# Performance work log

Hardware: AMD Instinct MI355X
Metric: run time of the kernel (lower is better)

The kernel has to match this reference:

```python
import jax, jax.numpy as jnp
import numpy as np
from jax import lax


def _binarize(t):
    # sign binarization to +1/-1 (zero maps to -1, matching torch.where(t > 0, 1, -1))
    return jnp.where(t > 0, 1.0, -1.0).astype(t.dtype)


def _bconv(x, w, b):
    # binary conv: binarize input and weights, then standard 3x3 'same' conv
    y = lax.conv_general_dilated(
        _binarize(x), _binarize(w),
        window_strides=(1, 1), padding=((1, 1), (1, 1)),
        dimension_numbers=('NCHW', 'OIHW', 'NCHW'))
    return y + b[None, :, None, None]


def _maxpool2(x):
    return lax.reduce_window(x, -jnp.inf, lax.max, (1, 1, 2, 2), (1, 1, 2, 2), 'VALID')


def setup_inputs() -> dict:
    key = jax.random.key(0)
    ks = jax.random.split(key, 13)
    s = 0.1
    return {
        'x': jax.random.normal(ks[0], (4096, 1, 28, 28), jnp.float32),
        'w1': jax.random.normal(ks[1], (32, 1, 3, 3), jnp.float32) * s,
        'b1': jax.random.normal(ks[2], (32,), jnp.float32) * s,
        'w2': jax.random.normal(ks[3], (64, 32, 3, 3), jnp.float32) * s,
        'b2': jax.random.normal(ks[4], (64,), jnp.float32) * s,
        'w3': jax.random.normal(ks[5], (16, 64, 3, 3), jnp.float32) * s,
        'b3': jax.random.normal(ks[6], (16,), jnp.float32) * s,
        'fc1_w': jax.random.normal(ks[7], (256, 16 * 7 * 7), jnp.float32) * s,
        'fc1_b': jax.random.normal(ks[8], (256,), jnp.float32) * s,
        'fc2_w': jax.random.normal(ks[9], (128, 256), jnp.float32) * s,
        'fc2_b': jax.random.normal(ks[10], (128,), jnp.float32) * s,
        'fc3_w': jax.random.normal(ks[11], (10, 128), jnp.float32) * s,
        'fc3_b': jax.random.normal(ks[12], (10,), jnp.float32) * s,
    }


def reference(x, w1, b1, w2, b2, w3, b3, fc1_w, fc1_b, fc2_w, fc2_b, fc3_w, fc3_b):
    h = jax.nn.relu(_maxpool2(_bconv(x, w1, b1)))      # [B,32,14,14]
    h = jax.nn.relu(_maxpool2(_bconv(h, w2, b2)))      # [B,64,7,7]
    h = jax.nn.relu(_bconv(h, w3, b3))                 # [B,16,7,7]
    h = h.reshape(-1, 16 * 7 * 7)
    h = jax.nn.relu(h @ fc1_w.T + fc1_b)
    h = jax.nn.relu(h @ fc2_w.T + fc2_b)
    return h @ fc3_w.T + fc3_b                          # [B,10]
```

## Files before the change

### kernel.cpp

```cpp
#include <hip/hip_runtime.h>
#include <cstdint>

#define OFF_PW    0
#define OFF_W1T   4096
#define OFF_W2T   823296
#define OFF_H3T   954368
#define OFF_H1T   14061568
#define OFF_H2T   18255872

__global__ __launch_bounds__(256) void prep(
    const float* __restrict__ w1, const float* __restrict__ w2,
    const float* __restrict__ w3,
    const float* __restrict__ fc1_w, const float* __restrict__ fc2_w,
    uint32_t* __restrict__ pw, float* __restrict__ w1T,
    float* __restrict__ w2T, float* __restrict__ h3T) {
    int idx = blockIdx.x * 256 + threadIdx.x;
    if (idx < 204800) {
        int k = idx >> 8, n = idx & 255;
        w1T[idx] = (k < 784) ? fc1_w[n * 784 + k] : 0.f;
        return;
    }
    idx -= 204800;
    if (idx < 32768) {
        int k = idx >> 7, n = idx & 127;
        w2T[idx] = fc2_w[n * 256 + k];
        return;
    }
    idx -= 32768;
    if (idx < 65536) {
        h3T[784 * 4096 + idx] = 0.f;
        return;
    }
    idx -= 65536;
    if (idx >= 896) return;
    if (idx < 32) {
        uint32_t b = 0;
#pragma unroll
        for (int k = 0; k < 9; ++k) b |= (w1[idx * 9 + k] > 0.f ? 1u : 0u) << k;
        pw[idx] = b;
    } else if (idx < 608) {
        int e = idx - 32;
        int oc = e / 9, tap = e - oc * 9;
        uint32_t b = 0;
#pragma unroll
        for (int ic = 0; ic < 32; ++ic)
            b |= (w2[(oc * 32 + ic) * 9 + tap] > 0.f ? 1u : 0u) << ic;
        pw[idx] = b;
    } else {
        int e = idx - 608;
        int oc = e / 18, r = e - oc * 18;
        int tap = r >> 1, half = r & 1;
        uint32_t b = 0;
#pragma unroll
        for (int ic = 0; ic < 32; ++ic)
            b |= (w3[(oc * 64 + half * 32 + ic) * 9 + tap] > 0.f ? 1u : 0u) << ic;
        pw[idx] = b;
    }
}

__device__ __forceinline__ uint32_t bfe3(uint32_t r, int j) { return (r >> j) & 7u; }

__global__ __launch_bounds__(256, 2) void conv_stack(
    const float* __restrict__ x, const float* __restrict__ b1,
    const float* __restrict__ b2, const float* __restrict__ b3,
    const uint32_t* __restrict__ pw, float* __restrict__ h3T) {
    __shared__ uint32_t s_xr[8 * 36];
    __shared__ uint32_t s_H1[8 * 260];
    __shared__ uint32_t s_H2[8 * 164];
    __shared__ uint32_t s_w1[32];
    __shared__ int s_sth1[32], s_ic1[32], s_ic2[64];
    __shared__ uint32_t s_W2t[576];
    __shared__ uint32_t s_W3t[288];
    __shared__ float s_b3[16];

    const int t = threadIdx.x;
    const int lane = t & 63;
    const int wid = t >> 6;
    const int img0 = blockIdx.x * 8;

    for (int i = t; i < 8 * 260; i += 256) s_H1[i] = 0;
    for (int i = t; i < 8 * 164; i += 256) s_H2[i] = 0;
    if (t < 224) {
        int im = t / 28, row = t - im * 28;
        const float4* xr = (const float4*)(x + (img0 + im) * 784 + row * 28);
        uint32_t b = 0;
#pragma unroll
        for (int q = 0; q < 7; ++q) {
            float4 v = xr[q];
            b |= (v.x > 0.f ? 1u : 0u) << (q * 4 + 0);
            b |= (v.y > 0.f ? 1u : 0u) << (q * 4 + 1);
            b |= (v.z > 0.f ? 1u : 0u) << (q * 4 + 2);
            b |= (v.w > 0.f ? 1u : 0u) << (q * 4 + 3);
        }
        s_xr[im * 36 + row] = b << 1;
    }
    if (t < 32) {
        s_w1[t] = pw[t];
        int ic = (int)floorf(-b1[t]) + 1;
        s_ic1[t] = ic;
        s_sth1[t] = (9 - ic) >> 1;
    } else if (t >= 32 && t < 96) {
        s_ic2[t - 32] = (int)floorf(-b2[t - 32]) + 1;
    } else if (t >= 96 && t < 112) {
        s_b3[t - 96] = b3[t - 96];
    }
    for (int i = t; i < 576; i += 256)
        s_W2t[i] = pw[32 + (i & 63) * 9 + (i >> 6)];
    for (int i = t; i < 288; i += 256)
        s_W3t[i] = pw[608 + (i & 15) * 18 + (i >> 4)];
    __syncthreads();

    for (int task = t; task < 1568; task += 256) {
        int pid = task >> 3, im = task & 7;
        int pi, pj;
        if (pid < 144) { pi = 1 + pid / 12; pj = 1 + pid - (pid / 12) * 12; }
        else {
            int b = pid - 144;
            if (b < 14)      { pi = 0;  pj = b; }
            else if (b < 28) { pi = 13; pj = b - 14; }
            else if (b < 40) { pi = 1 + (b - 28); pj = 0; }
            else             { pi = 1 + (b - 40); pj = 13; }
        }
        const uint32_t* xr = &s_xr[im * 36];
        int y0 = 2 * pi - 1;
        uint32_t r0 = (pi > 0)  ? xr[y0]     : 0u;
        uint32_t r1 = xr[y0 + 1];
        uint32_t r2 = xr[y0 + 2];
        uint32_t r3 = (pi < 13) ? xr[y0 + 3] : 0u;
        int j0 = 2 * pj, j1 = 2 * pj + 1;
        uint32_t s00 = bfe3(r0, j0) | (bfe3(r1, j0) << 3) | (bfe3(r2, j0) << 6);
        uint32_t s01 = bfe3(r0, j1) | (bfe3(r1, j1) << 3) | (bfe3(r2, j1) << 6);
        uint32_t s10 = bfe3(r1, j0) | (bfe3(r2, j0) << 3) | (bfe3(r3, j0) << 6);
        uint32_t s11 = bfe3(r1, j1) | (bfe3(r2, j1) << 3) | (bfe3(r3, j1) << 6);
        uint32_t word = 0;
        if (pid < 144) {
#pragma unroll
            for (int c = 0; c < 32; ++c) {
                uint32_t w = s_w1[c];
                int S = min(min(__popc(s00 ^ w), __popc(s01 ^ w)),
                            min(__popc(s10 ^ w), __popc(s11 ^ w)));
                word |= (uint32_t)(S <= s_sth1[c]) << c;
            }
        } else {
            uint32_t iT = (pi == 0)  ? 0x7u   : 0u;
            uint32_t iB = (pi == 13) ? 0x1C0u : 0u;
            uint32_t iL = (pj == 0)  ? 0x49u  : 0u;
            uint32_t iR = (pj == 13) ? 0x124u : 0u;
            uint32_t i00 = iT | iL, i01 = iT | iR, i10 = iB | iL, i11 = iB | iR;
            int n00 = 9 - __popc(i00), n01 = 9 - __popc(i01);
            int n10 = 9 - __popc(i10), n11 = 9 - __popc(i11);
#pragma unroll
            for (int c = 0; c < 32; ++c) {
                uint32_t w = s_w1[c];
                int v0 = n00 - 2 * (__popc(s00 ^ w) - __popc(w & i00));
                int v1 = n01 - 2 * (__popc(s01 ^ w) - __popc(w & i01));
                int v2 = n10 - 2 * (__popc(s10 ^ w) - __popc(w & i10));
                int v3 = n11 - 2 * (__popc(s11 ^ w) - __popc(w & i11));
                int vm = max(max(v0, v1), max(v2, v3));
                word |= (uint32_t)(vm >= s_ic1[c]) << c;
            }
        }
        s_H1[im * 260 + (pi + 1) * 16 + (pj + 1)] = word;
    }
    __syncthreads();

    {
        uint32_t w0 = s_W2t[0 * 64 + lane], w1r = s_W2t[1 * 64 + lane],
                 w2r = s_W2t[2 * 64 + lane], w3r = s_W2t[3 * 64 + lane],
                 w4 = s_W2t[4 * 64 + lane], w5 = s_W2t[5 * 64 + lane],
                 w6 = s_W2t[6 * 64 + lane], w7 = s_W2t[7 * 64 + lane],
                 w8 = s_W2t[8 * 64 + lane];
        int ic2 = s_ic2[lane];
        int sth2 = (288 - ic2) >> 1;
        int pc0 = __popc(w0), pc1 = __popc(w1r), pc2 = __popc(w2r);
        int pc3 = __popc(w3r), pc5 = __popc(w5), pc6 = __popc(w6);
        int pc7 = __popc(w7), pc8 = __popc(w8);
        int topc = pc0 + pc1 + pc2, botc = pc6 + pc7 + pc8;
        int lefc = pc0 + pc3 + pc6, rigc = pc2 + pc5 + pc8;

        for (int wt = wid; wt < 392; wt += 4) {
            int im = wt & 7, pos = wt >> 3;
            int pi, pj;
            if (pos < 25) { pi = 1 + pos / 5; pj = 1 + pos - (pos / 5) * 5; }
            else {
                int b = pos - 25;
                if (b < 7)       { pi = 0; pj = b; }
                else if (b < 14) { pi = 6; pj = b - 7; }
                else if (b < 19) { pi = b - 13; pj = 0; }
                else             { pi = b - 18; pj = 6; }
            }
            int base = im * 260 + 2 * pi * 16 + 2 * pj;
            uint2 ra0 = *(const uint2*)&s_H1[base],      ra1 = *(const uint2*)&s_H1[base + 2];
            uint2 rb0 = *(const uint2*)&s_H1[base + 16], rb1 = *(const uint2*)&s_H1[base + 18];
            uint2 rc0 = *(const uint2*)&s_H1[base + 32], rc1 = *(const uint2*)&s_H1[base + 34];
            uint2 rd0 = *(const uint2*)&s_H1[base + 48], rd1 = *(const uint2*)&s_H1[base + 50];
            uint32_t c00 = ra0.x, c01 = ra0.y, c02 = ra1.x, c03 = ra1.y;
            uint32_t c10 = rb0.x, c11 = rb0.y, c12 = rb1.x, c13 = rb1.y;
            uint32_t c20 = rc0.x, c21 = rc0.y, c22 = rc1.x, c23 = rc1.y;
            uint32_t c30 = rd0.x, c31 = rd0.y, c32 = rd1.x, c33 = rd1.y;
            int S00 = __popc(c00 ^ w0) + __popc(c01 ^ w1r) + __popc(c02 ^ w2r)
                    + __popc(c10 ^ w3r) + __popc(c11 ^ w4) + __popc(c12 ^ w5)
                    + __popc(c20 ^ w6) + __popc(c21 ^ w7) + __popc(c22 ^ w8);
            int S01 = __popc(c01 ^ w0) + __popc(c02 ^ w1r) + __popc(c03 ^ w2r)
                    + __popc(c11 ^ w3r) + __popc(c12 ^ w4) + __popc(c13 ^ w5)
                    + __popc(c21 ^ w6) + __popc(c22 ^ w7) + __popc(c23 ^ w8);
            int S10 = __popc(c10 ^ w0) + __popc(c11 ^ w1r) + __popc(c12 ^ w2r)
                    + __popc(c20 ^ w3r) + __popc(c21 ^ w4) + __popc(c22 ^ w5)
                    + __popc(c30 ^ w6) + __popc(c31 ^ w7) + __popc(c32 ^ w8);
            int S11 = __popc(c11 ^ w0) + __popc(c12 ^ w1r) + __popc(c13 ^ w2r)
                    + __popc(c21 ^ w3r) + __popc(c22 ^ w4) + __popc(c23 ^ w5)
                    + __popc(c31 ^ w6) + __popc(c32 ^ w7) + __popc(c33 ^ w8);
            int pred;
            if (pos < 25) {
                int Sm = min(min(S00, S01), min(S10, S11));
                pred = (Sm <= sth2);
            } else {
                int vmax;
                {
                    int rI = (pi == 0), cI = (pj == 0);
                    int corr = (rI ? topc : 0) + (cI ? lefc : 0) - ((rI & cI) ? pc0 : 0);
                    int nv = 32 * (9 - 3 * rI - 3 * cI + (rI & cI));
                    vmax = nv - 2 * (S00 - corr);
                }
                {
                    int rI = (pi == 0), cI = (pj == 6);
                    int corr = (rI ? topc : 0) + (cI ? rigc : 0) - ((rI & cI) ? pc2 : 0);
                    int nv = 32 * (9 - 3 * rI - 3 * cI + (rI & cI));
                    vmax = max(vmax, nv - 2 * (S01 - corr));
                }
                {
                    int rI = (pi == 6), cI = (pj == 0);
                    int corr = (rI ? botc : 0) + (cI ? lefc : 0) - ((rI & cI) ? pc6 : 0);
                    int nv = 32 * (9 - 3 * rI - 3 * cI + (rI & cI));
                    vmax = max(vmax, nv - 2 * (S10 - corr));
                }
                {
                    int rI = (pi == 6), cI = (pj == 6);
                    int corr = (rI ? botc : 0) + (cI ? rigc : 0) - ((rI & cI) ? pc8 : 0);
                    int nv = 32 * (9 - 3 * rI - 3 * cI + (rI & cI));
                    vmax = max(vmax, nv - 2 * (S11 - corr));
                }
                pred = (vmax >= ic2);
            }
            unsigned long long m = __ballot(pred);
            if (lane == 0) {
                *(uint2*)&s_H2[im * 164 + ((pi + 1) * 9 + (pj + 1)) * 2] =
                    make_uint2((uint32_t)m, (uint32_t)(m >> 32));
            }
        }
    }
    __syncthreads();

    {
        int oc = lane & 15, iq = lane >> 4;
        uint32_t w[18];
#pragma unroll
        for (int k = 0; k < 18; ++k) w[k] = s_W3t[k * 16 + oc];
        float bias3 = s_b3[oc];
        int pc[9];
#pragma unroll
        for (int k = 0; k < 9; ++k) pc[k] = __popc(w[2 * k]) + __popc(w[2 * k + 1]);
        int topc = pc[0] + pc[1] + pc[2], botc = pc[6] + pc[7] + pc[8];
        int lefc = pc[0] + pc[3] + pc[6], rigc = pc[2] + pc[5] + pc[8];

        for (int wt = wid; wt < 98; wt += 4) {
            int iq2 = wt & 1, pos = wt >> 1;
            int im = iq2 * 4 + iq;
            int pi, pj;
            if (pos < 25) { pi = 1 + pos / 5; pj = 1 + pos - (pos / 5) * 5; }
            else {
                int b = pos - 25;
                if (b < 7)       { pi = 0; pj = b; }
                else if (b < 14) { pi = 6; pj = b - 7; }
                else if (b < 19) { pi = b - 13; pj = 0; }
                else             { pi = b - 18; pj = 6; }
            }
            const uint32_t* hp = &s_H2[im * 164];
            int S = 0;
#pragma unroll
            for (int kh = 0; kh < 3; ++kh)
#pragma unroll
                for (int kw = 0; kw < 3; ++kw) {
                    uint2 cc = *(const uint2*)&hp[((pi + kh) * 9 + (pj + kw)) * 2];
                    int k = kh * 3 + kw;
                    S += __popc(cc.x ^ w[2 * k]) + __popc(cc.y ^ w[2 * k + 1]);
                }
            int v;
            if (pos < 25) {
                v = 576 - 2 * S;
            } else {
                int rT = (pi == 0), rB = (pi == 6), cL = (pj == 0), cR = (pj == 6);
                int rA = rT | rB, cA = cL | cR;
                int corr = (rT ? topc : 0) + (rB ? botc : 0) +
                           (cL ? lefc : 0) + (cR ? rigc : 0);
                if (rT & cL) corr -= pc[0];
                if (rT & cR) corr -= pc[2];
                if (rB & cL) corr -= pc[6];
                if (rB & cR) corr -= pc[8];
                int nInv = 3 * rA + 3 * cA - (rA & cA);
                v = 64 * (9 - nInv) - 2 * (S - corr);
            }
            float h = fmaxf((float)v + bias3, 0.f);
            h3T[(oc * 49 + pi * 7 + pj) * 4096 + img0 + im] = h;
        }
    }
}

__global__ __launch_bounds__(256, 2) void fc1_gemm(
    const float* __restrict__ aT, const float* __restrict__ bT,
    const float* __restrict__ bias, float* __restrict__ oT) {
    const int LDA = 68, LDB = 36;
    __shared__ float As[160 * LDA];
    __shared__ float Bs[160 * LDB];
    const int t = threadIdx.x;
    const int tx = t & 15, ty = t >> 4;
    const int img0 = blockIdx.x * 64;
    const int n0 = blockIdx.y * 32;
    float acc[4][2] = {{0.f}};

    for (int kc = 0; kc < 800; kc += 160) {
#pragma unroll
        for (int s = 0; s < 10; ++s) {
            int v = t + s * 256;
            int kk = v >> 4, q = (v & 15) * 4;
            *(float4*)&As[kk * LDA + q] =
                *(const float4*)&aT[(kc + kk) * 4096 + img0 + q];
        }
#pragma unroll
        for (int s = 0; s < 5; ++s) {
            int v = t + s * 256;
            int kk = v >> 3, q = (v & 7) * 4;
            *(float4*)&Bs[kk * LDB + q] =
                *(const float4*)&bT[(kc + kk) * 256 + n0 + q];
        }
        __syncthreads();
#pragma unroll 8
        for (int kk = 0; kk < 160; ++kk) {
            float4 a = *(const float4*)&As[kk * LDA + ty * 4];
            float2 b = *(const float2*)&Bs[kk * LDB + tx * 2];
            acc[0][0] += a.x * b.x; acc[0][1] += a.x * b.y;
            acc[1][0] += a.y * b.x; acc[1][1] += a.y * b.y;
            acc[2][0] += a.z * b.x; acc[2][1] += a.z * b.y;
            acc[3][0] += a.w * b.x; acc[3][1] += a.w * b.y;
        }
        __syncthreads();
    }
#pragma unroll
    for (int j = 0; j < 2; ++j) {
        int n = n0 + tx * 2 + j;
        float bj = bias[n];
        float4 ov;
        ov.x = fmaxf(acc[0][j] + bj, 0.f);
        ov.y = fmaxf(acc[1][j] + bj, 0.f);
        ov.z = fmaxf(acc[2][j] + bj, 0.f);
        ov.w = fmaxf(acc[3][j] + bj, 0.f);
        *(float4*)&oT[n * 4096 + img0 + ty * 4] = ov;
    }
}

__global__ __launch_bounds__(256, 2) void fc2_gemm(
    const float* __restrict__ aT, const float* __restrict__ bT,
    const float* __restrict__ bias, float* __restrict__ oT) {
    const int LD = 36;
    __shared__ float As[256 * LD];
    __shared__ float Bs[256 * LD];
    const int t = threadIdx.x;
    const int tx = t & 15, ty = t >> 4;
    const int img0 = blockIdx.x * 32;
    const int n0 = blockIdx.y * 32;
    float acc[2][2] = {{0.f}};

#pragma unroll
    for (int s = 0; s < 8; ++s) {
        int v = t + s * 256;
        int kk = v >> 3, q = (v & 7) * 4;
        *(float4*)&As[kk * LD + q] = *(const float4*)&aT[kk * 4096 + img0 + q];
        *(float4*)&Bs[kk * LD + q] = *(const float4*)&bT[kk * 128 + n0 + q];
    }
    __syncthreads();
#pragma unroll 8
    for (int kk = 0; kk < 256; ++kk) {
        float2 a = *(const float2*)&As[kk * LD + ty * 2];
        float2 b = *(const float2*)&Bs[kk * LD + tx * 2];
        acc[0][0] += a.x * b.x; acc[0][1] += a.x * b.y;
        acc[1][0] += a.y * b.x; acc[1][1] += a.y * b.y;
    }
#pragma unroll
    for (int j = 0; j < 2; ++j) {
        int n = n0 + tx * 2 + j;
        float bj = bias[n];
        float2 ov;
        ov.x = fmaxf(acc[0][j] + bj, 0.f);
        ov.y = fmaxf(acc[1][j] + bj, 0.f);
        *(float2*)&oT[n * 4096 + img0 + ty * 2] = ov;
    }
}

__global__ __launch_bounds__(256) void fc3_gemm(
    const float* __restrict__ aT, const float* __restrict__ w,
    const float* __restrict__ bias, float* __restrict__ out) {
    int id = blockIdx.x * 256 + threadIdx.x;
    int n = id >> 12, img = id & 4095;
    const float* wr = w + n * 128;
    float a0 = 0.f, a1 = 0.f, a2 = 0.f, a3 = 0.f;
#pragma unroll 8
    for (int k = 0; k < 128; k += 4) {
        a0 += aT[(k + 0) * 4096 + img] * wr[k + 0];
        a1 += aT[(k + 1) * 4096 + img] * wr[k + 1];
        a2 += aT[(k + 2) * 4096 + img] * wr[k + 2];
        a3 += aT[(k + 3) * 4096 + img] * wr[k + 3];
    }
    out[img * 10 + n] = (a0 + a1) + (a2 + a3) + bias[n];
}

extern "C" void kernel_launch(void* const* d_in, const int* in_sizes, int n_in,
                              void* d_out, int out_size, void* d_ws, size_t ws_size,
                              hipStream_t stream) {
    const float* x     = (const float*)d_in[0];
    const float* w1    = (const float*)d_in[1];
    const float* b1    = (const float*)d_in[2];
    const float* w2    = (const float*)d_in[3];
    const float* b2    = (const float*)d_in[4];
    const float* w3    = (const float*)d_in[5];
    const float* b3    = (const float*)d_in[6];
    const float* fc1_w = (const float*)d_in[7];
    const float* fc1_b = (const float*)d_in[8];
    const float* fc2_w = (const float*)d_in[9];
    const float* fc2_b = (const float*)d_in[10];
    const float* fc3_w = (const float*)d_in[11];
    const float* fc3_b = (const float*)d_in[12];
    float* out = (float*)d_out;

    const int B = in_sizes[0] / 784;
    char* ws = (char*)d_ws;
    uint32_t* pw = (uint32_t*)(ws + OFF_PW);
    float* w1T = (float*)(ws + OFF_W1T);
    float* w2T = (float*)(ws + OFF_W2T);
    float* h3T = (float*)(ws + OFF_H3T);
    float* h1T = (float*)(ws + OFF_H1T);
    float* h2T = (float*)(ws + OFF_H2T);

    hipLaunchKernelGGL(prep, dim3(1188), dim3(256), 0, stream,
                       w1, w2, w3, fc1_w, fc2_w, pw, w1T, w2T, h3T);
    hipLaunchKernelGGL(conv_stack, dim3(B / 8), dim3(256), 0, stream,
                       x, b1, b2, b3, pw, h3T);
    hipLaunchKernelGGL(fc1_gemm, dim3(B / 64, 8), dim3(256), 0, stream,
                       h3T, w1T, fc1_b, h1T);
    hipLaunchKernelGGL(fc2_gemm, dim3(B / 32, 4), dim3(256), 0, stream,
                       h1T, w2T, fc2_b, h2T);
    hipLaunchKernelGGL(fc3_gemm, dim3(B * 10 / 256), dim3(256), 0, stream,
                       h2T, fc3_w, fc3_b, out);
}
```

Baseline: 224.9 us.

## Restructure conv stack per-image and split-K FC GEMMs with fused bias/ReLU epilogues

The conv stack now handles 4 images per block with one wavefront per image in layer 2. That wave loads whole H1 rows into registers and sweeps all 7 columns, replacing the per-position gather, and occupancy is raised to 4 blocks per CU. fc1 and fc2 become larger-register-tile split-K GEMMs that write partial sums into extra workspace buffers, or use atomics when the workspace is too small. The partial reduction, bias and ReLU are folded into the next layer's load. This aims to raise parallelism and data reuse in the GEMMs, but it adds partial-buffer traffic and a workspace-size-dependent code path.

After: 224.4 us. No clear change (-0.2%).

```diff
diff --git a/kernel.cpp b/kernel.cpp
--- a/kernel.cpp
+++ b/kernel.cpp
@@ -7,6 +7,9 @@
 #define OFF_H3T   954368
 #define OFF_H1T   14061568
 #define OFF_H2T   18255872
+#define OFF_H1EXT 20353024ull
+#define OFF_H2EXT 32935936ull
+#define WS_NEED_EXT 35033088ull
 
 __global__ __launch_bounds__(256) void prep(
     const float* __restrict__ w1, const float* __restrict__ w2,
@@ -60,28 +63,42 @@
 
 __device__ __forceinline__ uint32_t bfe3(uint32_t r, int j) { return (r >> j) & 7u; }
 
-__global__ __launch_bounds__(256, 2) void conv_stack(
+__global__ __launch_bounds__(256, 4) void conv_stack(
     const float* __restrict__ x, const float* __restrict__ b1,
     const float* __restrict__ b2, const float* __restrict__ b3,
     const uint32_t* __restrict__ pw, float* __restrict__ h3T) {
-    __shared__ uint32_t s_xr[8 * 36];
-    __shared__ uint32_t s_H1[8 * 260];
-    __shared__ uint32_t s_H2[8 * 164];
+    __shared__ __align__(16) uint32_t s_H1[4][16][16];
+    __shared__ __align__(16) uint32_t s_H2[4][9][9][2];
+    __shared__ uint32_t s_xr[4][32];
     __shared__ uint32_t s_w1[32];
     __shared__ int s_sth1[32], s_ic1[32], s_ic2[64];
-    __shared__ uint32_t s_W2t[576];
-    __shared__ uint32_t s_W3t[288];
+    __shared__ uint32_t s_W2t[9][64];
+    __shared__ uint32_t s_W3t[18][16];
     __shared__ float s_b3[16];
 
     const int t = threadIdx.x;
     const int lane = t & 63;
     const int wid = t >> 6;
-    const int img0 = blockIdx.x * 8;
-
-    for (int i = t; i < 8 * 260; i += 256) s_H1[i] = 0;
-    for (int i = t; i < 8 * 164; i += 256) s_H2[i] = 0;
-    if (t < 224) {
-        int im = t / 28, row = t - im * 28;
+    const int img0 = blockIdx.x * 4;
+
+    {
+        uint32_t* h1f = &s_H1[0][0][0];
+        for (int i = t; i < 1024; i += 256) h1f[i] = 0;
+        uint32_t* h2f = &s_H2[0][0][0][0];
+        for (int i = t; i < 648; i += 256) h2f[i] = 0;
+    }
+    if (t < 32) {
+        s_w1[t] = pw[t];
+        int ic = (int)floorf(-b1[t]) + 1;
+        s_ic1[t] = ic;
+        s_sth1[t] = (9 - ic) >> 1;
+    } else if (t < 96) {
+        s_ic2[t - 32] = (int)floorf(-b2[t - 32]) + 1;
+    } else if (t < 112) {
+        s_b3[t - 96] = b3[t - 96];
+    } else if (t >= 128 && t < 240) {
+        int r = t - 128;
+        int im = r / 28, row = r - im * 28;
         const float4* xr = (const float4*)(x + (img0 + im) * 784 + row * 28);
         uint32_t b = 0;
 #pragma unroll
@@ -92,26 +109,16 @@
             b |= (v.z > 0.f ? 1u : 0u) << (q * 4 + 2);
             b |= (v.w > 0.f ? 1u : 0u) << (q * 4 + 3);
         }
-        s_xr[im * 36 + row] = b << 1;
-    }
-    if (t < 32) {
-        s_w1[t] = pw[t];
-        int ic = (int)floorf(-b1[t]) + 1;
-        s_ic1[t] = ic;
-        s_sth1[t] = (9 - ic) >> 1;
-    } else if (t >= 32 && t < 96) {
-        s_ic2[t - 32] = (int)floorf(-b2[t - 32]) + 1;
-    } else if (t >= 96 && t < 112) {
-        s_b3[t - 96] = b3[t - 96];
+        s_xr[im][row] = b << 1;
     }
     for (int i = t; i < 576; i += 256)
-        s_W2t[i] = pw[32 + (i & 63) * 9 + (i >> 6)];
+        s_W2t[i >> 6][i & 63] = pw[32 + (i & 63) * 9 + (i >> 6)];
     for (int i = t; i < 288; i += 256)
-        s_W3t[i] = pw[608 + (i & 15) * 18 + (i >> 4)];
+        s_W3t[i >> 4][i & 15] = pw[608 + (i & 15) * 18 + (i >> 4)];
     __syncthreads();
 
-    for (int task = t; task < 1568; task += 256) {
-        int pid = task >> 3, im = task & 7;
+    for (int task = t; task < 784; task += 256) {
+        int im = task & 3, pid = task >> 2;
         int pi, pj;
         if (pid < 144) { pi = 1 + pid / 12; pj = 1 + pid - (pid / 12) * 12; }
         else {
@@ -121,7 +128,7 @@
             else if (b < 40) { pi = 1 + (b - 28); pj = 0; }
             else             { pi = 1 + (b - 40); pj = 13; }
         }
-        const uint32_t* xr = &s_xr[im * 36];
+        const uint32_t* xr = &s_xr[im][0];
         int y0 = 2 * pi - 1;
         uint32_t r0 = (pi > 0)  ? xr[y0]     : 0u;
         uint32_t r1 = xr[y0 + 1];
@@ -134,7 +141,7 @@
         uint32_t s11 = bfe3(r1, j1) | (bfe3(r2, j1) << 3) | (bfe3(r3, j1) << 6);
         uint32_t word = 0;
         if (pid < 144) {
-#pragma unroll
+#pragma unroll 4
             for (int c = 0; c < 32; ++c) {
                 uint32_t w = s_w1[c];
                 int S = min(min(__popc(s00 ^ w), __popc(s01 ^ w)),
@@ -149,7 +156,7 @@
             uint32_t i00 = iT | iL, i01 = iT | iR, i10 = iB | iL, i11 = iB | iR;
             int n00 = 9 - __popc(i00), n01 = 9 - __popc(i01);
             int n10 = 9 - __popc(i10), n11 = 9 - __popc(i11);
-#pragma unroll
+#pragma unroll 4
             for (int c = 0; c < 32; ++c) {
                 uint32_t w = s_w1[c];
                 int v0 = n00 - 2 * (__popc(s00 ^ w) - __popc(w & i00));
@@ -160,102 +167,102 @@
                 word |= (uint32_t)(vm >= s_ic1[c]) << c;
             }
         }
-        s_H1[im * 260 + (pi + 1) * 16 + (pj + 1)] = word;
+        s_H1[im][pi + 1][pj + 1] = word;
     }
     __syncthreads();
 
     {
-        uint32_t w0 = s_W2t[0 * 64 + lane], w1r = s_W2t[1 * 64 + lane],
-                 w2r = s_W2t[2 * 64 + lane], w3r = s_W2t[3 * 64 + lane],
-                 w4 = s_W2t[4 * 64 + lane], w5 = s_W2t[5 * 64 + lane],
-                 w6 = s_W2t[6 * 64 + lane], w7 = s_W2t[7 * 64 + lane],
-                 w8 = s_W2t[8 * 64 + lane];
+        const int im = wid;
+        uint32_t wv[9];
+#pragma unroll
+        for (int k = 0; k < 9; ++k) wv[k] = s_W2t[k][lane];
         int ic2 = s_ic2[lane];
         int sth2 = (288 - ic2) >> 1;
-        int pc0 = __popc(w0), pc1 = __popc(w1r), pc2 = __popc(w2r);
-        int pc3 = __popc(w3r), pc5 = __popc(w5), pc6 = __popc(w6);
-        int pc7 = __popc(w7), pc8 = __popc(w8);
-        int topc = pc0 + pc1 + pc2, botc = pc6 + pc7 + pc8;
-        int lefc = pc0 + pc3 + pc6, rigc = pc2 + pc5 + pc8;
-
-        for (int wt = wid; wt < 392; wt += 4) {
-            int im = wt & 7, pos = wt >> 3;
-            int pi, pj;
-            if (pos < 25) { pi = 1 + pos / 5; pj = 1 + pos - (pos / 5) * 5; }
-            else {
-                int b = pos - 25;
-                if (b < 7)       { pi = 0; pj = b; }
-                else if (b < 14) { pi = 6; pj = b - 7; }
-                else if (b < 19) { pi = b - 13; pj = 0; }
-                else             { pi = b - 18; pj = 6; }
+        int pc0 = __popc(wv[0]), pc2 = __popc(wv[2]);
+        int pc6 = __popc(wv[6]), pc8 = __popc(wv[8]);
+        int topc = pc0 + __popc(wv[1]) + pc2;
+        int botc = pc6 + __popc(wv[7]) + pc8;
+        int lefc = pc0 + __popc(wv[3]) + pc6;
+        int rigc = pc2 + __popc(wv[5]) + pc8;
+        const uint32_t* plane = &s_H1[im][0][0];
+
+        for (int pi = 0; pi < 7; ++pi) {
+            uint32_t C[4][16];
+#pragma unroll
+            for (int r = 0; r < 4; ++r) {
+                const uint32_t* rp = &plane[(2 * pi + r) * 16];
+                *(uint4*)&C[r][0]  = *(const uint4*)&rp[0];
+                *(uint4*)&C[r][4]  = *(const uint4*)&rp[4];
+                *(uint4*)&C[r][8]  = *(const uint4*)&rp[8];
+                *(uint4*)&C[r][12] = *(const uint4*)&rp[12];
             }
-            int base = im * 260 + 2 * pi * 16 + 2 * pj;
-            uint2 ra0 = *(const uint2*)&s_H1[base],      ra1 = *(const uint2*)&s_H1[base + 2];
-            uint2 rb0 = *(const uint2*)&s_H1[base + 16], rb1 = *(const uint2*)&s_H1[base + 18];
-            uint2 rc0 = *(const uint2*)&s_H1[base + 32], rc1 = *(const uint2*)&s_H1[base + 34];
-            uint2 rd0 = *(const uint2*)&s_H1[base + 48], rd1 = *(const uint2*)&s_H1[base + 50];
-            uint32_t c00 = ra0.x, c01 = ra0.y, c02 = ra1.x, c03 = ra1.y;
-            uint32_t c10 = rb0.x, c11 = rb0.y, c12 = rb1.x, c13 = rb1.y;
-            uint32_t c20 = rc0.x, c21 = rc0.y, c22 = rc1.x, c23 = rc1.y;
-            uint32_t c30 = rd0.x, c31 = rd0.y, c32 = rd1.x, c33 = rd1.y;
-            int S00 = __popc(c00 ^ w0) + __popc(c01 ^ w1r) + __popc(c02 ^ w2r)
-                    + __popc(c10 ^ w3r) + __popc(c11 ^ w4) + __popc(c12 ^ w5)
-                    + __popc(c20 ^ w6) + __popc(c21 ^ w7) + __popc(c22 ^ w8);
-            int S01 = __popc(c01 ^ w0) + __popc(c02 ^ w1r) + __popc(c03 ^ w2r)
-                    + __popc(c11 ^ w3r) + __popc(c12 ^ w4) + __popc(c13 ^ w5)
-                    + __popc(c21 ^ w6) + __popc(c22 ^ w7) + __popc(c23 ^ w8);
-            int S10 = __popc(c10 ^ w0) + __popc(c11 ^ w1r) + __popc(c12 ^ w2r)
-                    + __popc(c20 ^ w3r) + __popc(c21 ^ w4) + __popc(c22 ^ w5)
-                    + __popc(c30 ^ w6) + __popc(c31 ^ w7) + __popc(c32 ^ w8);
-            int S11 = __popc(c11 ^ w0) + __popc(c12 ^ w1r) + __popc(c13 ^ w2r)
-                    + __popc(c21 ^ w3r) + __popc(c22 ^ w4) + __popc(c23 ^ w5)
-                    + __popc(c31 ^ w6) + __popc(c32 ^ w7) + __popc(c33 ^ w8);
-            int pred;
-            if (pos < 25) {
-                int Sm = min(min(S00, S01), min(S10, S11));
-                pred = (Sm <= sth2);
-            } else {
-                int vmax;
-                {
-                    int rI = (pi == 0), cI = (pj == 0);
-                    int corr = (rI ? topc : 0) + (cI ? lefc : 0) - ((rI & cI) ? pc0 : 0);
-                    int nv = 32 * (9 - 3 * rI - 3 * cI + (rI & cI));
-                    vmax = nv - 2 * (S00 - corr);
+            const int rT = (pi == 0), rB = (pi == 6);
+#pragma unroll
+            for (int pj = 0; pj < 7; ++pj) {
+                int S00 = 0, S01 = 0, S10 = 0, S11 = 0;
+#pragma unroll
+                for (int kh = 0; kh < 3; ++kh)
+#pragma unroll
+                    for (int kw = 0; kw < 3; ++kw) {
+                        uint32_t ww = wv[kh * 3 + kw];
+                        S00 += __popc(C[kh][2 * pj + kw] ^ ww);
+                        S01 += __popc(C[kh][2 * pj + 1 + kw] ^ ww);
+                        S10 += __popc(C[kh + 1][2 * pj + kw] ^ ww);
+                        S11 += __popc(C[kh + 1][2 * pj + 1 + kw] ^ ww);
+                    }
+                int pred;
+                if (pj >= 1 && pj <= 5) {
+                    if (!rT && !rB) {
+                        int Sm = min(min(S00, S01), min(S10, S11));
+                        pred = (Sm <= sth2);
+                    } else if (rT) {
+                        int v0 = 192 - 2 * (S00 - topc);
+                        int v1 = 192 - 2 * (S01 - topc);
+                        int v2 = 288 - 2 * S10;
+                        int v3 = 288 - 2 * S11;
+                        pred = (max(max(v0, v1), max(v2, v3)) >= ic2);
+                    } else {
+                        int v0 = 288 - 2 * S00;
+                        int v1 = 288 - 2 * S01;
+                        int v2 = 192 - 2 * (S10 - botc);
+                        int v3 = 192 - 2 * (S11 - botc);
+                        pred = (max(max(v0, v1), max(v2, v3)) >= ic2);
+                    }
+                } else {
+                    const int cL = (pj == 0), cR = (pj == 6);
+                    int v0, v1, v2, v3;
+                    { int rI = rT, cI = cL;
+                      int corr = (rI ? topc : 0) + (cI ? lefc : 0) - ((rI & cI) ? pc0 : 0);
+                      int nv = 32 * (9 - 3 * rI - 3 * cI + (rI & cI));
+                      v0 = nv - 2 * (S00 - corr); }
+                    { int rI = rT, cI = cR;
+                      int corr = (rI ? topc : 0) + (cI ? rigc : 0) - ((rI & cI) ? pc2 : 0);
+                      int nv = 32 * (9 - 3 * rI - 3 * cI + (rI & cI));
+                      v1 = nv - 2 * (S01 - corr); }
+                    { int rI = rB, cI = cL;
+                      int corr = (rI ? botc : 0) + (cI ? lefc : 0) - ((rI & cI) ? pc6 : 0);
+                      int nv = 32 * (9 - 3 * rI - 3 * cI + (rI & cI));
+                      v2 = nv - 2 * (S10 - corr); }
+                    { int rI = rB, cI = cR;
+                      int corr = (rI ? botc : 0) + (cI ? rigc : 0) - ((rI & cI) ? pc8 : 0);
+                      int nv = 32 * (9 - 3 * rI - 3 * cI + (rI & cI));
+                      v3 = nv - 2 * (S11 - corr); }
+                    pred = (max(max(v0, v1), max(v2, v3)) >= ic2);
                 }
-                {
-                    int rI = (pi == 0), cI = (pj == 6);
-                    int corr = (rI ? topc : 0) + (cI ? rigc : 0) - ((rI & cI) ? pc2 : 0);
-                    int nv = 32 * (9 - 3 * rI - 3 * cI + (rI & cI));
-                    vmax = max(vmax, nv - 2 * (S01 - corr));
-                }
-                {
-                    int rI = (pi == 6), cI = (pj == 0);
-                    int corr = (rI ? botc : 0) + (cI ? lefc : 0) - ((rI & cI) ? pc6 : 0);
-                    int nv = 32 * (9 - 3 * rI - 3 * cI + (rI & cI));
-                    vmax = max(vmax, nv - 2 * (S10 - corr));
-                }
-                {
-                    int rI = (pi == 6), cI = (pj == 6);
-                    int corr = (rI ? botc : 0) + (cI ? rigc : 0) - ((rI & cI) ? pc8 : 0);
-                    int nv = 32 * (9 - 3 * rI - 3 * cI + (rI & cI));
-                    vmax = max(vmax, nv - 2 * (S11 - corr));
-                }
-                pred = (vmax >= ic2);
+                unsigned long long m = __ballot(pred);
+                if (lane == 0)
+                    *(uint2*)&s_H2[im][pi + 1][pj + 1][0] =
+                        make_uint2((uint32_t)m, (uint32_t)(m >> 32));
             }
-            unsigned long long m = __ballot(pred);
-            if (lane == 0) {
-                *(uint2*)&s_H2[im * 164 + ((pi + 1) * 9 + (pj + 1)) * 2] =
-                    make_uint2((uint32_t)m, (uint32_t)(m >> 32));
-            }
         }
     }
     __syncthreads();
 
     {
-        int oc = lane & 15, iq = lane >> 4;
+        int oc = lane & 15, im = lane >> 4;
         uint32_t w[18];
 #pragma unroll
-        for (int k = 0; k < 18; ++k) w[k] = s_W3t[k * 16 + oc];
+        for (int k = 0; k < 18; ++k) w[k] = s_W3t[k][oc];
         float bias3 = s_b3[oc];
         int pc[9];
 #pragma unroll
@@ -263,30 +270,19 @@
         int topc = pc[0] + pc[1] + pc[2], botc = pc[6] + pc[7] + pc[8];
         int lefc = pc[0] + pc[3] + pc[6], rigc = pc[2] + pc[5] + pc[8];
 
-        for (int wt = wid; wt < 98; wt += 4) {
-            int iq2 = wt & 1, pos = wt >> 1;
-            int im = iq2 * 4 + iq;
-            int pi, pj;
-            if (pos < 25) { pi = 1 + pos / 5; pj = 1 + pos - (pos / 5) * 5; }
-            else {
-                int b = pos - 25;
-                if (b < 7)       { pi = 0; pj = b; }
-                else if (b < 14) { pi = 6; pj = b - 7; }
-                else if (b < 19) { pi = b - 13; pj = 0; }
-                else             { pi = b - 18; pj = 6; }
-            }
-            const uint32_t* hp = &s_H2[im * 164];
+        for (int pos = wid; pos < 49; pos += 4) {
+            int pi = pos / 7, pj = pos - pi * 7;
             int S = 0;
 #pragma unroll
             for (int kh = 0; kh < 3; ++kh)
 #pragma unroll
                 for (int kw = 0; kw < 3; ++kw) {
-                    uint2 cc = *(const uint2*)&hp[((pi + kh) * 9 + (pj + kw)) * 2];
+                    uint2 cc = *(const uint2*)&s_H2[im][pi + kh][pj + kw][0];
                     int k = kh * 3 + kw;
                     S += __popc(cc.x ^ w[2 * k]) + __popc(cc.y ^ w[2 * k + 1]);
                 }
             int v;
-            if (pos < 25) {
+            if (pi >= 1 && pi <= 5 && pj >= 1 && pj <= 5) {
                 v = 576 - 2 * S;
             } else {
                 int rT = (pi == 0), rB = (pi == 6), cL = (pj == 0), cR = (pj == 6);
@@ -301,116 +297,170 @@
                 v = 64 * (9 - nInv) - 2 * (S - corr);
             }
             float h = fmaxf((float)v + bias3, 0.f);
-            h3T[(oc * 49 + pi * 7 + pj) * 4096 + img0 + im] = h;
+            h3T[(oc * 49 + pos) * 4096 + img0 + im] = h;
         }
     }
 }
 
-__global__ __launch_bounds__(256, 2) void fc1_gemm(
+__global__ __launch_bounds__(128, 2) void fc1_gemm(
     const float* __restrict__ aT, const float* __restrict__ bT,
-    const float* __restrict__ bias, float* __restrict__ oT) {
-    const int LDA = 68, LDB = 36;
-    __shared__ float As[160 * LDA];
-    __shared__ float Bs[160 * LDB];
+    float* __restrict__ p0, float* __restrict__ pext, int bufmode) {
+    __shared__ __align__(16) float As[40][64];
+    __shared__ __align__(16) float Bs[40][128];
     const int t = threadIdx.x;
+    const int img0 = blockIdx.x * 64;
+    const int n0 = blockIdx.y * 128;
+    const int z = blockIdx.z;
+    const int k0 = z * 200;
     const int tx = t & 15, ty = t >> 4;
+    float acc[8][8] = {{0.f}};
+
+    for (int ch = 0; ch < 5; ++ch) {
+        int kb = k0 + ch * 40;
+#pragma unroll
+        for (int s = 0; s < 5; ++s) {
+            int fid = t + s * 128;
+            int kk = fid >> 4, c4 = (fid & 15) * 4;
+            *(float4*)&As[kk][c4] = *(const float4*)&aT[(kb + kk) * 4096 + img0 + c4];
+        }
+#pragma unroll
+        for (int s = 0; s < 10; ++s) {
+            int fid = t + s * 128;
+            int kk = fid >> 5, c4 = (fid & 31) * 4;
+            *(float4*)&Bs[kk][c4] = *(const float4*)&bT[(kb + kk) * 256 + n0 + c4];
+        }
+        __syncthreads();
+#pragma unroll 4
+        for (int kk = 0; kk < 40; ++kk) {
+            float4 a0 = *(const float4*)&As[kk][ty * 8];
+            float4 a1 = *(const float4*)&As[kk][ty * 8 + 4];
+            float4 b0 = *(const float4*)&Bs[kk][tx * 8];
+            float4 b1 = *(const float4*)&Bs[kk][tx * 8 + 4];
+            float av[8] = {a0.x, a0.y, a0.z, a0.w, a1.x, a1.y, a1.z, a1.w};
+            float bv[8] = {b0.x, b0.y, b0.z, b0.w, b1.x, b1.y, b1.z, b1.w};
+#pragma unroll
+            for (int i = 0; i < 8; ++i)
+#pragma unroll
+                for (int j = 0; j < 8; ++j) acc[i][j] += av[i] * bv[j];
+        }
+        __syncthreads();
+    }
+    if (bufmode) {
+        float* dst = (z == 0) ? p0 : pext + (size_t)(z - 1) * 1048576;
+#pragma unroll
+        for (int j = 0; j < 8; ++j) {
+            float* d = &dst[(n0 + tx * 8 + j) * 4096 + img0 + ty * 8];
+            float4 v0 = make_float4(acc[0][j], acc[1][j], acc[2][j], acc[3][j]);
+            float4 v1 = make_float4(acc[4][j], acc[5][j], acc[6][j], acc[7][j]);
+            *(float4*)&d[0] = v0;
+            *(float4*)&d[4] = v1;
+        }
+    } else {
+#pragma unroll
+        for (int j = 0; j < 8; ++j) {
+            float* d = &p0[(n0 + tx * 8 + j) * 4096 + img0 + ty * 8];
+#pragma unroll
+            for (int i = 0; i < 8; ++i) atomicAdd(&d[i], acc[i][j]);
+        }
+    }
+}
+
+__global__ __launch_bounds__(256, 2) void fc2_gemm(
+    const float* __restrict__ p0, const float* __restrict__ pext,
+    const float* __restrict__ fc1_b,
+    const float* __restrict__ bT,
+    float* __restrict__ q0, float* __restrict__ qext, int bufmode) {
+    __shared__ __align__(16) float As[32][64];
+    __shared__ __align__(16) float Bs[32][64];
+    const int t = threadIdx.x;
     const int img0 = blockIdx.x * 64;
-    const int n0 = blockIdx.y * 32;
-    float acc[4][2] = {{0.f}};
-
-    for (int kc = 0; kc < 800; kc += 160) {
-#pragma unroll
-        for (int s = 0; s < 10; ++s) {
-            int v = t + s * 256;
-            int kk = v >> 4, q = (v & 15) * 4;
-            *(float4*)&As[kk * LDA + q] =
-                *(const float4*)&aT[(kc + kk) * 4096 + img0 + q];
-        }
-#pragma unroll
-        for (int s = 0; s < 5; ++s) {
-            int v = t + s * 256;
-            int kk = v >> 3, q = (v & 7) * 4;
-            *(float4*)&Bs[kk * LDB + q] =
-                *(const float4*)&bT[(kc + kk) * 256 + n0 + q];
+    const int n0 = blockIdx.y * 64;
+    const int z = blockIdx.z;
+    const int k0 = z * 128;
+    const int tx = t & 15, ty = t >> 4;
+    float acc[4][4] = {{0.f}};
+
+    for (int ch = 0; ch < 4; ++ch) {
+        int kb = k0 + ch * 32;
+        {
+            int kk = t >> 3, c4 = (t & 7) * 8;
+            size_t off = (size_t)(kb + kk) * 4096 + img0 + c4;
+            float4 v0 = *(const float4*)&p0[off];
+            float4 v1 = *(const float4*)&p0[off + 4];
+            if (bufmode) {
+#pragma unroll
+                for (int s = 0; s < 3; ++s) {
+                    const float* pp = pext + (size_t)s * 1048576;
+                    float4 u0 = *(const float4*)&pp[off];
+                    float4 u1 = *(const float4*)&pp[off + 4];
+                    v0.x += u0.x; v0.y += u0.y; v0.z += u0.z; v0.w += u0.w;
+                    v1.x += u1.x; v1.y += u1.y; v1.z += u1.z; v1.w += u1.w;
+                }
+            }
+            float bb = fc1_b[kb + kk];
+            v0.x = fmaxf(v0.x + bb, 0.f); v0.y = fmaxf(v0.y + bb, 0.f);
+            v0.z = fmaxf(v0.z + bb, 0.f); v0.w = fmaxf(v0.w + bb, 0.f);
+            v1.x = fmaxf(v1.x + bb, 0.f); v1.y = fmaxf(v1.y + bb, 0.f);
+            v1.z = fmaxf(v1.z + bb, 0.f); v1.w = fmaxf(v1.w + bb, 0.f);
+            *(float4*)&As[kk][c4] = v0;
+            *(float4*)&As[kk][c4 + 4] = v1;
+            *(float4*)&Bs[kk][c4] = *(const float4*)&bT[(kb + kk) * 128 + n0 + c4];
+            *(float4*)&Bs[kk][c4 + 4] = *(const float4*)&bT[(kb + kk) * 128 + n0 + c4 + 4];
         }
         __syncthreads();
 #pragma unroll 8
-        for (int kk = 0; kk < 160; ++kk) {
-            float4 a = *(const float4*)&As[kk * LDA + ty * 4];
-            float2 b = *(const float2*)&Bs[kk * LDB + tx * 2];
-            acc[0][0] += a.x * b.x; acc[0][1] += a.x * b.y;
-            acc[1][0] += a.y * b.x; acc[1][1] += a.y * b.y;
-            acc[2][0] += a.z * b.x; acc[2][1] += a.z * b.y;
-            acc[3][0] += a.w * b.x; acc[3][1] += a.w * b.y;
+        for (int kk = 0; kk < 32; ++kk) {
+            float4 a = *(const float4*)&As[kk][ty * 4];
+            float4 b = *(const float4*)&Bs[kk][tx * 4];
+            float av[4] = {a.x, a.y, a.z, a.w};
+            float bv[4] = {b.x, b.y, b.z, b.w};
+#pragma unroll
+            for (int i = 0; i < 4; ++i)
+#pragma unroll
+                for (int j = 0; j < 4; ++j) acc[i][j] += av[i] * bv[j];
         }
         __syncthreads();
     }
-#pragma unroll
-    for (int j = 0; j < 2; ++j) {
-        int n = n0 + tx * 2 + j;
-        float bj = bias[n];
-        float4 ov;
-        ov.x = fmaxf(acc[0][j] + bj, 0.f);
-        ov.y = fmaxf(acc[1][j] + bj, 0.f);
-        ov.z = fmaxf(acc[2][j] + bj, 0.f);
-        ov.w = fmaxf(acc[3][j] + bj, 0.f);
-        *(float4*)&oT[n * 4096 + img0 + ty * 4] = ov;
+    if (bufmode) {
+        float* dst = (z == 0) ? q0 : qext;
+#pragma unroll
+        for (int j = 0; j < 4; ++j) {
+            float4 v = make_float4(acc[0][j], acc[1][j], acc[2][j], acc[3][j]);
+            *(float4*)&dst[(n0 + tx * 4 + j) * 4096 + img0 + ty * 4] = v;
+        }
+    } else {
+#pragma unroll
+        for (int j = 0; j < 4; ++j) {
+            float* d = &q0[(n0 + tx * 4 + j) * 4096 + img0 + ty * 4];
+#pragma unroll
+            for (int i = 0; i < 4; ++i) atomicAdd(&d[i], acc[i][j]);
+        }
     }
 }
 
-__global__ __launch_bounds__(256, 2) void fc2_gemm(
-    const float* __restrict__ aT, const float* __restrict__ bT,
-    const float* __restrict__ bias, float* __restrict__ oT) {
-    const int LD = 36;
-    __shared__ float As[256 * LD];
-    __shared__ float Bs[256 * LD];
-    const int t = threadIdx.x;
-    const int tx = t & 15, ty = t >> 4;
-    const int img0 = blockIdx.x * 32;
-    const int n0 = blockIdx.y * 32;
-    float acc[2][2] = {{0.f}};
-
-#pragma unroll
-    for (int s = 0; s < 8; ++s) {
-        int v = t + s * 256;
-        int kk = v >> 3, q = (v & 7) * 4;
-        *(float4*)&As[kk * LD + q] = *(const float4*)&aT[kk * 4096 + img0 + q];
-        *(float4*)&Bs[kk * LD + q] = *(const float4*)&bT[kk * 128 + n0 + q];
-    }
-    __syncthreads();
-#pragma unroll 8
-    for (int kk = 0; kk < 256; ++kk) {
-        float2 a = *(const float2*)&As[kk * LD + ty * 2];
-        float2 b = *(const float2*)&Bs[kk * LD + tx * 2];
-        acc[0][0] += a.x * b.x; acc[0][1] += a.x * b.y;
-        acc[1][0] += a.y * b.x; acc[1][1] += a.y * b.y;
-    }
-#pragma unroll
-    for (int j = 0; j < 2; ++j) {
-        int n = n0 + tx * 2 + j;
-        float bj = bias[n];
-        float2 ov;
-        ov.x = fmaxf(acc[0][j] + bj, 0.f);
-        ov.y = fmaxf(acc[1][j] + bj, 0.f);
-        *(float2*)&oT[n * 4096 + img0 + ty * 2] = ov;
-    }
-}
-
 __global__ __launch_bounds__(256) void fc3_gemm(
-    const float* __restrict__ aT, const float* __restrict__ w,
-    const float* __restrict__ bias, float* __restrict__ out) {
+    const float* __restrict__ q0, const float* __restrict__ qext,
+    const float* __restrict__ fc2_b,
+    const float* __restrict__ w, const float* __restrict__ bias,
+    float* __restrict__ out, int bufmode) {
     int id = blockIdx.x * 256 + threadIdx.x;
     int n = id >> 12, img = id & 4095;
     const float* wr = w + n * 128;
-    float a0 = 0.f, a1 = 0.f, a2 = 0.f, a3 = 0.f;
+    float a0 = 0.f, a1 = 0.f;
 #pragma unroll 8
-    for (int k = 0; k < 128; k += 4) {
-        a0 += aT[(k + 0) * 4096 + img] * wr[k + 0];
-        a1 += aT[(k + 1) * 4096 + img] * wr[k + 1];
-        a2 += aT[(k + 2) * 4096 + img] * wr[k + 2];
-        a3 += aT[(k + 3) * 4096 + img] * wr[k + 3];
-    }
-    out[img * 10 + n] = (a0 + a1) + (a2 + a3) + bias[n];
+    for (int k = 0; k < 128; k += 2) {
+        float v0 = q0[(k + 0) * 4096 + img];
+        float v1 = q0[(k + 1) * 4096 + img];
+        if (bufmode) {
+            v0 += qext[(k + 0) * 4096 + img];
+            v1 += qext[(k + 1) * 4096 + img];
+        }
+        v0 = fmaxf(v0 + fc2_b[k], 0.f);
+        v1 = fmaxf(v1 + fc2_b[k + 1], 0.f);
+        a0 += v0 * wr[k];
+        a1 += v1 * wr[k + 1];
+    }
+    out[img * 10 + n] = a0 + a1 + bias[n];
 }
 
 extern "C" void kernel_launch(void* const* d_in, const int* in_sizes, int n_in,
@@ -437,17 +487,24 @@
     float* w1T = (float*)(ws + OFF_W1T);
     float* w2T = (float*)(ws + OFF_W2T);
     float* h3T = (float*)(ws + OFF_H3T);
-    float* h1T = (float*)(ws + OFF_H1T);
-    float* h2T = (float*)(ws + OFF_H2T);
-
+    float* h1p0 = (float*)(ws + OFF_H1T);
+    float* h2p0 = (float*)(ws + OFF_H2T);
+    const int bufmode = (ws_size >= WS_NEED_EXT) ? 1 : 0;
+    float* h1ext = bufmode ? (float*)(ws + OFF_H1EXT) : h1p0;
+    float* h2ext = bufmode ? (float*)(ws + OFF_H2EXT) : h2p0;
+
+    if (!bufmode) {
+        hipMemsetAsync(h1p0, 0, 4194304, stream);
+        hipMemsetAsync(h2p0, 0, 2097152, stream);
+    }
     hipLaunchKernelGGL(prep, dim3(1188), dim3(256), 0, stream,
                        w1, w2, w3, fc1_w, fc2_w, pw, w1T, w2T, h3T);
-    hipLaunchKernelGGL(conv_stack, dim3(B / 8), dim3(256), 0, stream,
+    hipLaunchKernelGGL(conv_stack, dim3(B / 4), dim3(256), 0, stream,
                        x, b1, b2, b3, pw, h3T);
-    hipLaunchKernelGGL(fc1_gemm, dim3(B / 64, 8), dim3(256), 0, stream,
-                       h3T, w1T, fc1_b, h1T);
-    hipLaunchKernelGGL(fc2_gemm, dim3(B / 32, 4), dim3(256), 0, stream,
-                       h1T, w2T, fc2_b, h2T);
+    hipLaunchKernelGGL(fc1_gemm, dim3(B / 64, 2, 4), dim3(128), 0, stream,
+                       h3T, w1T, h1p0, h1ext, bufmode);
+    hipLaunchKernelGGL(fc2_gemm, dim3(B / 64, 2, 2), dim3(256), 0, stream,
+                       h1p0, h1ext, fc1_b, w2T, h2p0, h2ext, bufmode);
     hipLaunchKernelGGL(fc3_gemm, dim3(B * 10 / 256), dim3(256), 0, stream,
-                       h2T, fc3_w, fc3_b, out);
+                       h2p0, h2ext, fc2_b, fc3_w, fc3_b, out, bufmode);
 }
```
